# Kernel tuning notes

Measured on AMD Instinct MI355X. Metric: run time of the kernel, lower is better.

The kernel has to match this reference:

```python
import jax, jax.numpy as jnp
import numpy as np

B, N, C, H = 4, 2048, 1024, 16
D = C // H  # dim_per_head = 64
NEG = -1e9  # stands in for -inf masked_fill (finite to keep grads clean)


def setup_inputs() -> dict:
    key0 = jax.random.key(0)
    ks = jax.random.split(key0, 12)
    inp = {
        "query": jax.random.normal(ks[0], (B, N, C), dtype=jnp.float32),
        "key": jax.random.normal(ks[1], (B, N, C), dtype=jnp.float32),
        "value": jax.random.normal(ks[2], (B, N, C), dtype=jnp.float32),
        "ratio": jax.random.uniform(ks[3], (B, N), dtype=jnp.float32),
        "attn_mask": jax.random.randint(ks[4], (B, N, N), 0, 2) == 1,
        # learned params (Linear layers are bias-free; weights stored as [in, out])
        "Wq": jax.random.normal(ks[5], (C, C), dtype=jnp.float32) / np.sqrt(C),
        "Wk": jax.random.normal(ks[6], (C, C), dtype=jnp.float32) / np.sqrt(C),
        "Wv": jax.random.normal(ks[7], (C, C), dtype=jnp.float32) / np.sqrt(C),
        "Wo": jax.random.normal(ks[8], (C, C), dtype=jnp.float32) / np.sqrt(C),
        "gamma": jnp.ones((C,), dtype=jnp.float32),
        "beta": jnp.zeros((C,), dtype=jnp.float32),
    }
    return inp


def reference(query, key, value, ratio, attn_mask, Wq, Wk, Wv, Wo, gamma, beta):
    residual = query
    # projections -> [B, H, N, D]
    q = (query @ Wq).reshape(B, N, H, D).transpose(0, 2, 1, 3)
    k = (key @ Wk).reshape(B, N, H, D).transpose(0, 2, 1, 3)
    v = (value @ Wv).reshape(B, N, H, D).transpose(0, 2, 1, 3)

    scale = D ** (-0.5)
    scores = jnp.einsum("bhid,bhjd->bhij", q, k) * scale  # [B,H,N1,N2]
    scores = jnp.where(attn_mask[:, None, :, :], NEG, scores)
    scores = scores * ratio[:, None, None, :]  # ratio broadcast over heads & queries
    # NON-STANDARD: softmax over dim=2 (the QUERY axis), faithful to source
    attn = jax.nn.softmax(scores, axis=2)
    # dropout omitted (eval mode)
    ctx = jnp.einsum("bhij,bhjd->bhid", attn, v)  # [B,H,N1,D]
    ctx = ctx.transpose(0, 2, 1, 3).reshape(B, N, C)
    out = ctx @ Wo
    x = residual + out
    # LayerNorm over last dim
    mu = jnp.mean(x, axis=-1, keepdims=True)
    var = jnp.var(x, axis=-1, keepdims=True)
    xn = (x - mu) * jax.lax.rsqrt(var + 1e-5)
    return xn * gamma + beta
```

## Files before the change

kernel.cpp:

```cpp
#include <hip/hip_runtime.h>
#include <hip/hip_bf16.h>
#include <stdint.h>

#define BB 4
#define NN 2048
#define CC 1024
#define HH 16
#define DD 64

typedef __attribute__((ext_vector_type(8))) short bf16x8;
typedef __attribute__((ext_vector_type(4))) float f32x4;

#define LOG2E 1.44269504088896f

__device__ __forceinline__ float exp2_hw(float x) {
  float r;
  asm("v_exp_f32 %0, %1" : "=v"(r) : "v"(x));
  return r;
}
#define EXP2(x) exp2_hw(x)

__device__ __forceinline__ unsigned short f2bf(float x) {
  uint32_t u = __float_as_uint(x);
  uint32_t r = (u + 0x7FFFu + ((u >> 16) & 1u)) >> 16;
  return (unsigned short)r;
}
__device__ __forceinline__ float bf2f(unsigned short v) {
  return __uint_as_float(((uint32_t)v) << 16);
}
__device__ __forceinline__ float load_in_f(const void* p, size_t idx, int f32in) {
  if (f32in) return ((const float*)p)[idx];
  return bf2f(((const uint16_t*)p)[idx]);
}
__device__ __forceinline__ void gload16(uint16_t* lds_base, const uint16_t* gsrc) {
  __builtin_amdgcn_global_load_lds(
      (const __attribute__((address_space(1))) uint32_t*)(const void*)gsrc,
      (__attribute__((address_space(3))) uint32_t*)(void*)lds_base,
      16, 0, 0);
}

__global__ void detect_kernel(const uint32_t* __restrict__ q,
                              const uint32_t* __restrict__ m,
                              int* __restrict__ flags) {
  if (threadIdx.x == 0 && blockIdx.x == 0) {
    int sane = 0;
    for (int i = 0; i < 128; ++i) {
      uint32_t w = q[i];
      int e0 = (int)((w >> 7) & 0xFFu);
      int e1 = (int)((w >> 23) & 0xFFu);
      sane += (e0 >= 0x70 && e0 <= 0x8F) ? 1 : 0;
      sane += (e1 >= 0x70 && e1 <= 0x8F) ? 1 : 0;
    }
    flags[0] = (sane >= 208) ? 0 : 1;
    int allsmall = 1;
    for (int i = 0; i < 16; ++i) if (m[i] > 1u) allsmall = 0;
    flags[1] = allsmall;
  }
}

__global__ void conv_bf16_3(const void* __restrict__ s0, const void* __restrict__ s1,
                            const void* __restrict__ s2,
                            uint16_t* __restrict__ d0, uint16_t* __restrict__ d1,
                            uint16_t* __restrict__ d2,
                            int n, const int* __restrict__ flags) {
  const int f32in = flags[0];
  const void* src = (blockIdx.z == 0) ? s0 : (blockIdx.z == 1) ? s1 : s2;
  uint16_t* dst = (blockIdx.z == 0) ? d0 : (blockIdx.z == 1) ? d1 : d2;
  int idx = blockIdx.x * blockDim.x + threadIdx.x;
  const int total = n >> 2;
  const int stride = gridDim.x * blockDim.x;
  if (f32in) {
    const float4* s = (const float4*)src;
    for (; idx < total; idx += stride) {
      float4 v = s[idx];
      ushort4 o;
      o.x = f2bf(v.x); o.y = f2bf(v.y); o.z = f2bf(v.z); o.w = f2bf(v.w);
      ((ushort4*)dst)[idx] = o;
    }
  } else {
    const ushort4* s = (const ushort4*)src;
    for (; idx < total; idx += stride) ((ushort4*)dst)[idx] = s[idx];
  }
}

__global__ void conv_ratio2(const void* __restrict__ src, float* __restrict__ rs,
                            float* __restrict__ ng, int n, const int* __restrict__ flags) {
  const int f32in = flags[0];
  int idx = blockIdx.x * blockDim.x + threadIdx.x;
  const int stride = gridDim.x * blockDim.x;
  for (; idx < n; idx += stride) {
    float r = load_in_f(src, idx, f32in);
    rs[idx] = r * 0.125f * LOG2E;
    ng[idx] = r * (-1e9f) * LOG2E;
  }
}

__global__ void conv_maskbits(const void* __restrict__ src, uint32_t* __restrict__ dst,
                              int n, const int* __restrict__ flags) {
  const int isint = flags[1];
  const int gw = (blockIdx.x * blockDim.x + threadIdx.x) >> 6;
  const int lane = threadIdx.x & 63;
  const int nw = (gridDim.x * blockDim.x) >> 6;
  const int totalw = n >> 6;
  for (int w = gw; w < totalw; w += nw) {
    int e = w * 64 + lane;
    bool m;
    if (isint) m = (((const int*)src)[e] != 0);
    else       m = (((const uint8_t*)src)[e] != 0);
    unsigned long long bal = __ballot(m);
    if (lane == 0) ((unsigned long long*)dst)[w] = bal;
  }
}

__global__ __launch_bounds__(256)
void transW(const void* w0, const void* w1, const void* w2, const void* w3,
            uint16_t* __restrict__ wt, const int* __restrict__ flags) {
  const int f32in = flags[0];
  const void* src = (blockIdx.z == 0) ? w0 : (blockIdx.z == 1) ? w1
                   : (blockIdx.z == 2) ? w2 : w3;
  uint16_t* dst = wt + (size_t)blockIdx.z * CC * CC;
  __shared__ float t[32][33];
  const int tx = threadIdx.x, ty = threadIdx.y;
  const int n0 = blockIdx.x * 32, k0 = blockIdx.y * 32;
#pragma unroll
  for (int r = 0; r < 4; ++r) {
    int k = k0 + ty + r * 8;
    t[ty + r * 8][tx] = load_in_f(src, (size_t)k * CC + n0 + tx, f32in);
  }
  __syncthreads();
#pragma unroll
  for (int r = 0; r < 4; ++r) {
    int n = n0 + ty + r * 8;
    dst[(size_t)n * CC + k0 + tx] = f2bf(t[tx][ty + r * 8]);
  }
}

__global__ __launch_bounds__(256, 2)
void gemmQKV(const uint16_t* __restrict__ xq, const uint16_t* __restrict__ xk,
             const uint16_t* __restrict__ xv, const uint16_t* __restrict__ Wt,
             uint16_t* __restrict__ qb, uint16_t* __restrict__ kb,
             uint16_t* __restrict__ vtb, const float* __restrict__ rowscale) {
  __shared__ uint16_t As[128 * 32];
  __shared__ uint16_t Bs[128 * 32];
  const int tid = threadIdx.x;
  const int wid = tid >> 6, lane = tid & 63;
  const int g = lane >> 4, c = lane & 15;
  const int n0g = blockIdx.y * 128;
  const int sel = n0g >> 10;
  const int n0 = n0g & 1023;
  const int m0 = blockIdx.x * 128;
  const uint16_t* A = (sel == 0) ? xq : (sel == 1) ? xk : xv;
  const uint16_t* Bt = Wt + (size_t)sel * CC * CC;
  const int wr = wid >> 1, wc = wid & 1;
  f32x4 acc[4][4] = {};
  for (int k0 = 0; k0 < 1024; k0 += 32) {
    __syncthreads();
#pragma unroll
    for (int is = 0; is < 2; ++is) {
      int sb = is * 256 + wid * 64;
      int s = sb + lane;
      int r = s >> 2, kp = s & 3;
      int kps = kp ^ ((r >> 1) & 3);
      gload16(&As[sb * 8], A + (size_t)(m0 + r) * 1024 + k0 + kps * 8);
      gload16(&Bs[sb * 8], Bt + (size_t)(n0 + r) * 1024 + k0 + kps * 8);
    }
    __syncthreads();
    bf16x8 a[4], b[4];
#pragma unroll
    for (int mi = 0; mi < 4; ++mi) {
      int row = wr * 64 + mi * 16 + c;
      a[mi] = *(const bf16x8*)&As[row * 32 + (g ^ ((row >> 1) & 3)) * 8];
    }
#pragma unroll
    for (int ni = 0; ni < 4; ++ni) {
      int row = wc * 64 + ni * 16 + c;
      b[ni] = *(const bf16x8*)&Bs[row * 32 + (g ^ ((row >> 1) & 3)) * 8];
    }
#pragma unroll
    for (int mi = 0; mi < 4; ++mi)
#pragma unroll
      for (int ni = 0; ni < 4; ++ni)
        acc[mi][ni] = __builtin_amdgcn_mfma_f32_16x16x32_bf16(a[mi], b[ni], acc[mi][ni], 0, 0, 0);
  }
  float rsv[4][4];
  if (sel == 1) {
#pragma unroll
    for (int mi = 0; mi < 4; ++mi)
#pragma unroll
      for (int r = 0; r < 4; ++r)
        rsv[mi][r] = rowscale[m0 + wr * 64 + mi * 16 + g * 4 + r];
  }
#pragma unroll
  for (int mi = 0; mi < 4; ++mi)
#pragma unroll
    for (int ni = 0; ni < 4; ++ni)
#pragma unroll
      for (int r = 0; r < 4; ++r) {
        int mrow = m0 + wr * 64 + mi * 16 + g * 4 + r;
        int ncol = n0 + wc * 64 + ni * 16 + c;
        float v = acc[mi][ni][r];
        int b_ = mrow >> 11, i = mrow & 2047, h = ncol >> 6, d = ncol & 63;
        if (sel == 0) {
          qb[((size_t)(b_ * 16 + h) * 2048 + i) * 64 + d] = f2bf(v);
        } else if (sel == 1) {
          kb[((size_t)(b_ * 16 + h) * 2048 + i) * 64 + d] = f2bf(v * rsv[mi][r]);
        } else {
          vtb[((size_t)(b_ * 16 + h) * 64 + d) * 2048 + i] = f2bf(v);
        }
      }
}

__global__ __launch_bounds__(256, 2)
void gemmO(const uint16_t* __restrict__ A, const uint16_t* __restrict__ Bt,
           float* __restrict__ out, const void* __restrict__ resid,
           const int* __restrict__ flags) {
  __shared__ uint16_t As[128 * 32];
  __shared__ uint16_t Bs[128 * 32];
  const int tid = threadIdx.x;
  const int wid = tid >> 6, lane = tid & 63;
  const int g = lane >> 4, c = lane & 15;
  const int m0 = blockIdx.x * 128, n0 = blockIdx.y * 128;
  const int wr = wid >> 1, wc = wid & 1;
  f32x4 acc[4][4] = {};
  for (int k0 = 0; k0 < 1024; k0 += 32) {
    __syncthreads();
#pragma unroll
    for (int is = 0; is < 2; ++is) {
      int sb = is * 256 + wid * 64;
      int s = sb + lane;
      int r = s >> 2, kp = s & 3;
      int kps = kp ^ ((r >> 1) & 3);
      gload16(&As[sb * 8], A + (size_t)(m0 + r) * 1024 + k0 + kps * 8);
      gload16(&Bs[sb * 8], Bt + (size_t)(n0 + r) * 1024 + k0 + kps * 8);
    }
    __syncthreads();
    bf16x8 a[4], b[4];
#pragma unroll
    for (int mi = 0; mi < 4; ++mi) {
      int row = wr * 64 + mi * 16 + c;
      a[mi] = *(const bf16x8*)&As[row * 32 + (g ^ ((row >> 1) & 3)) * 8];
    }
#pragma unroll
    for (int ni = 0; ni < 4; ++ni) {
      int row = wc * 64 + ni * 16 + c;
      b[ni] = *(const bf16x8*)&Bs[row * 32 + (g ^ ((row >> 1) & 3)) * 8];
    }
#pragma unroll
    for (int mi = 0; mi < 4; ++mi)
#pragma unroll
      for (int ni = 0; ni < 4; ++ni)
        acc[mi][ni] = __builtin_amdgcn_mfma_f32_16x16x32_bf16(a[mi], b[ni], acc[mi][ni], 0, 0, 0);
  }
  const int f32in = flags[0];
#pragma unroll
  for (int mi = 0; mi < 4; ++mi)
#pragma unroll
    for (int ni = 0; ni < 4; ++ni)
#pragma unroll
      for (int r = 0; r < 4; ++r) {
        int mrow = m0 + wr * 64 + mi * 16 + g * 4 + r;
        int ncol = n0 + wc * 64 + ni * 16 + c;
        size_t idx = (size_t)mrow * 1024 + ncol;
        out[idx] = acc[mi][ni][r] + load_in_f(resid, idx, f32in);
      }
}

__global__ __launch_bounds__(256, 2)
void attn_stats(const uint16_t* __restrict__ qb, const uint16_t* __restrict__ kb,
                uint16_t* __restrict__ vt, const uint32_t* __restrict__ mbits,
                const float* __restrict__ ngbuf) {
  __shared__ float redL[4][128];
  __shared__ float invsh[128];
  const int tid = threadIdx.x, wid = tid >> 6, lane = tid & 63;
  const int g = lane >> 4, c = lane & 15;
  const int bh = blockIdx.x, b_ = bh >> 4;
  const int j0 = blockIdx.y * 128;
  const uint16_t* Kg = kb + (size_t)bh * NN * DD + (size_t)j0 * DD;
  const uint16_t* Qg = qb + (size_t)bh * NN * DD;
  const uint32_t* Mrow = mbits + (size_t)b_ * NN * 64 + (j0 >> 5);
  bf16x8 kf[2][8];
#pragma unroll
  for (int ks = 0; ks < 2; ++ks)
#pragma unroll
    for (int nj = 0; nj < 8; ++nj)
      kf[ks][nj] = *(const bf16x8*)(Kg + (size_t)(nj * 16 + c) * 64 + ks * 32 + g * 8);
  float ng8[8], l_[8];
#pragma unroll
  for (int nj = 0; nj < 8; ++nj) {
    ng8[nj] = ngbuf[b_ * NN + j0 + nj * 16 + c];
    l_[nj] = 0.f;
  }
  bf16x8 qa[2][2], qn[2][2];
  uint4 mqa[8], mqb[8];
#pragma unroll
  for (int ks = 0; ks < 2; ++ks)
#pragma unroll
    for (int mi = 0; mi < 2; ++mi)
      qa[ks][mi] = *(const bf16x8*)(Qg + (size_t)(wid * 32 + mi * 16 + c) * 64 + ks * 32 + g * 8);
#pragma unroll
  for (int u = 0; u < 8; ++u) {
    int mi = u >> 2, r = u & 3;
    mqa[u] = *(const uint4*)(Mrow + (size_t)(wid * 32 + mi * 16 + g * 4 + r) * 64);
  }

  auto body = [&](bf16x8 (&qc)[2][2], bf16x8 (&qp)[2][2],
                  uint4 (&mc)[8], uint4 (&mn)[8], int i0) {
    f32x4 sacc[2][8] = {};
    __builtin_amdgcn_s_setprio(1);
#pragma unroll
    for (int ks = 0; ks < 2; ++ks)
#pragma unroll
      for (int mi = 0; mi < 2; ++mi)
#pragma unroll
        for (int nj = 0; nj < 8; ++nj)
          sacc[mi][nj] = __builtin_amdgcn_mfma_f32_16x16x32_bf16(qc[ks][mi], kf[ks][nj], sacc[mi][nj], 0, 0, 0);
    __builtin_amdgcn_s_setprio(0);
    int ip = (i0 + 128) & (NN - 1);
#pragma unroll
    for (int ks = 0; ks < 2; ++ks)
#pragma unroll
      for (int mi = 0; mi < 2; ++mi)
        qp[ks][mi] = *(const bf16x8*)(Qg + (size_t)(ip + wid * 32 + mi * 16 + c) * 64 + ks * 32 + g * 8);
#pragma unroll
    for (int u = 0; u < 8; ++u) {
      int mi = u >> 2, r = u & 3;
      mn[u] = *(const uint4*)(Mrow + (size_t)(ip + wid * 32 + mi * 16 + g * 4 + r) * 64);
    }
#pragma unroll
    for (int mi = 0; mi < 2; ++mi)
#pragma unroll
      for (int r = 0; r < 4; ++r) {
        const uint4 mw = mc[mi * 4 + r];
#pragma unroll
        for (int nj = 0; nj < 8; ++nj) {
          uint32_t w = (nj < 2) ? mw.x : (nj < 4) ? mw.y : (nj < 6) ? mw.z : mw.w;
          bool bit = (w >> ((nj & 1) * 16 + c)) & 1u;
          float se = bit ? ng8[nj] : sacc[mi][nj][r];
          l_[nj] += EXP2(se);
        }
      }
  };
  for (int it = 0; it < 8; ++it) {
    body(qa, qn, mqa, mqb, it * 256);
    body(qn, qa, mqb, mqa, it * 256 + 128);
  }
#pragma unroll
  for (int nj = 0; nj < 8; ++nj) {
    float l = l_[nj];
    l += __shfl_xor(l, 16);
    l += __shfl_xor(l, 32);
    if (g == 0) redL[wid][nj * 16 + c] = l;
  }
  __syncthreads();
  if (tid < 128) {
    float L = redL[0][tid] + redL[1][tid] + redL[2][tid] + redL[3][tid];
    invsh[tid] = 1.0f / L;
  }
  __syncthreads();
  {
    const int d = tid >> 2, jseg = (tid & 3) * 32;
    uint16_t* vrow = vt + (size_t)bh * DD * NN + (size_t)d * NN + j0 + jseg;
#pragma unroll
    for (int u = 0; u < 4; ++u) {
      bf16x8 v = *(const bf16x8*)(vrow + u * 8);
      bf16x8 o;
#pragma unroll
      for (int e = 0; e < 8; ++e) {
        float f = bf2f((unsigned short)v[e]) * invsh[jseg + u * 8 + e];
        o[e] = (short)f2bf(f);
      }
      *(bf16x8*)(vrow + u * 8) = o;
    }
  }
}

__global__ __launch_bounds__(256, 3)
void attn_pv(const uint16_t* __restrict__ qb, const uint16_t* __restrict__ kb,
             const uint16_t* __restrict__ vt, const uint32_t* __restrict__ mbits,
             const float* __restrict__ ngbuf, uint16_t* __restrict__ ctxr) {
  __shared__ uint16_t Ks[2][64 * 64];
  __shared__ uint16_t Vs[2][64 * 64];
  __shared__ uint16_t Ps[128 * 64];
  const int tid = threadIdx.x, wid = tid >> 6, lane = tid & 63;
  const int g = lane >> 4, c = lane & 15;
  const int bh = blockIdx.x, b_ = bh >> 4, h = bh & 15;
  const int i0 = blockIdx.y * 128;
  const uint16_t* Qg = qb + (size_t)bh * NN * DD;
  const uint16_t* Kg = kb + (size_t)bh * NN * DD;
  const uint16_t* Vg = vt + (size_t)bh * DD * NN;
  const uint32_t* Mb = mbits + (size_t)b_ * NN * 64;
  const float* ngb = ngbuf + b_ * NN;

  auto stageK = [&](int buf, int j0) {
#pragma unroll
    for (int is = 0; is < 2; ++is) {
      int sb = is * 256 + wid * 64;
      int s = sb + lane;
      int row = s >> 3, gr = s & 7;
      gload16(&Ks[buf][sb * 8], Kg + (size_t)(j0 + row) * 64 + (gr ^ (row & 7)) * 8);
    }
  };
  auto stageV = [&](int buf, int j0) {
#pragma unroll
    for (int is = 0; is < 2; ++is) {
      int sb = is * 256 + wid * 64;
      int s = sb + lane;
      int d = s >> 3, gr = s & 7;
      gload16(&Vs[buf][sb * 8], Vg + (size_t)d * NN + j0 + (gr ^ (d & 7)) * 8);
    }
  };

  bf16x8 qf[2][2];
#pragma unroll
  for (int ks = 0; ks < 2; ++ks)
#pragma unroll
    for (int mi = 0; mi < 2; ++mi)
      qf[ks][mi] = *(const bf16x8*)(Qg + (size_t)(i0 + wid * 32 + mi * 16 + c) * 64 + ks * 32 + g * 8);

  stageK(0, 0); stageV(0, 0);
  __syncthreads();

  f32x4 cacc[2][4] = {};
  for (int t = 0; t < 32; ++t) {
    const int j0 = t * 64, cb = t & 1, nb = cb ^ 1;
    if (t < 31) { stageK(nb, j0 + 64); stageV(nb, j0 + 64); }
    uint2 mw0 = *(const uint2*)(Mb + (size_t)(i0 + wid * 32 + c) * 64 + (j0 >> 5));
    uint2 mw1 = *(const uint2*)(Mb + (size_t)(i0 + wid * 32 + 16 + c) * 64 + (j0 >> 5));
    float4 ngv[4];
#pragma unroll
    for (int nj = 0; nj < 4; ++nj)
      ngv[nj] = *(const float4*)(ngb + j0 + nj * 16 + g * 4);
    f32x4 st[4][2] = {};
    __builtin_amdgcn_s_setprio(1);
#pragma unroll
    for (int ks = 0; ks < 2; ++ks) {
      bf16x8 kfr[4];
#pragma unroll
      for (int nj = 0; nj < 4; ++nj) {
        int row = nj * 16 + c;
        kfr[nj] = *(const bf16x8*)&Ks[cb][row * 64 + (((ks * 4 + g) ^ (c & 7))) * 8];
      }
#pragma unroll
      for (int nj = 0; nj < 4; ++nj)
#pragma unroll
        for (int mi = 0; mi < 2; ++mi)
          st[nj][mi] = __builtin_amdgcn_mfma_f32_16x16x32_bf16(kfr[nj], qf[ks][mi], st[nj][mi], 0, 0, 0);
    }
    __builtin_amdgcn_s_setprio(0);
    uint2 pkv[4][2];
#pragma unroll
    for (int nj = 0; nj < 4; ++nj) {
      const float4 ngq = ngv[nj];
      float nz[4] = {ngq.x, ngq.y, ngq.z, ngq.w};
#pragma unroll
      for (int mi = 0; mi < 2; ++mi) {
        const uint2 mw = mi ? mw1 : mw0;
        uint32_t w = (nj < 2) ? mw.x : mw.y;
        float p[4];
#pragma unroll
        for (int u = 0; u < 4; ++u) {
          bool bit = (w >> ((nj & 1) * 16 + g * 4 + u)) & 1u;
          float se = bit ? nz[u] : st[nj][mi][u];
          p[u] = EXP2(se);
        }
        uint32_t lo, hi;
        asm("v_cvt_pk_bf16_f32 %0, %1, %2" : "=v"(lo) : "v"(p[0]), "v"(p[1]));
        asm("v_cvt_pk_bf16_f32 %0, %1, %2" : "=v"(hi) : "v"(p[2]), "v"(p[3]));
        pkv[nj][mi] = make_uint2(lo, hi);
      }
    }
#pragma unroll
    for (int nj = 0; nj < 4; ++nj)
#pragma unroll
      for (int mi = 0; mi < 2; ++mi) {
        int iL = wid * 32 + mi * 16 + c;
        int gran = (nj * 2 + (g >> 1)) ^ (c & 7);
        *(uint2*)((char*)Ps + iL * 128 + gran * 16 + (g & 1) * 8) = pkv[nj][mi];
      }
    __syncthreads();
    __builtin_amdgcn_s_setprio(1);
#pragma unroll
    for (int ks = 0; ks < 2; ++ks) {
      bf16x8 pa[2], vb[4];
#pragma unroll
      for (int mi = 0; mi < 2; ++mi) {
        int row = wid * 32 + mi * 16 + c;
        pa[mi] = *(const bf16x8*)((const char*)Ps + row * 128 + (((ks * 4 + g) ^ (c & 7))) * 16);
      }
#pragma unroll
      for (int nd = 0; nd < 4; ++nd) {
        int row = nd * 16 + c;
        vb[nd] = *(const bf16x8*)&Vs[cb][row * 64 + (((ks * 4 + g) ^ (c & 7))) * 8];
      }
#pragma unroll
      for (int mi = 0; mi < 2; ++mi)
#pragma unroll
        for (int nd = 0; nd < 4; ++nd)
          cacc[mi][nd] = __builtin_amdgcn_mfma_f32_16x16x32_bf16(pa[mi], vb[nd], cacc[mi][nd], 0, 0, 0);
    }
    __builtin_amdgcn_s_setprio(0);
    __syncthreads();
  }
#pragma unroll
  for (int mi = 0; mi < 2; ++mi)
#pragma unroll
    for (int nd = 0; nd < 4; ++nd)
#pragma unroll
      for (int r = 0; r < 4; ++r) {
        int i = i0 + wid * 32 + mi * 16 + g * 4 + r;
        int d = nd * 16 + c;
        ctxr[((size_t)(b_ * NN + i)) * CC + h * DD + d] = f2bf(cacc[mi][nd][r]);
      }
}

__global__ __launch_bounds__(256)
void ln_kernel(const float* __restrict__ xbuf, const void* __restrict__ gamma,
               const void* __restrict__ beta, float* __restrict__ out,
               const int* __restrict__ flags) {
  const int row = blockIdx.x;
  const int tid = threadIdx.x;
  const float4 v = ((const float4*)(xbuf + (size_t)row * CC))[tid];
  float s = v.x + v.y + v.z + v.w;
  float s2 = v.x * v.x + v.y * v.y + v.z * v.z + v.w * v.w;
#pragma unroll
  for (int off = 32; off >= 1; off >>= 1) {
    s += __shfl_xor(s, off);
    s2 += __shfl_xor(s2, off);
  }
  __shared__ float red[8];
  const int wid = tid >> 6, lane = tid & 63;
  if (lane == 0) { red[wid] = s; red[4 + wid] = s2; }
  __syncthreads();
  float ts = red[0] + red[1] + red[2] + red[3];
  float ts2 = red[4] + red[5] + red[6] + red[7];
  float mu = ts * (1.f / 1024.f);
  float var = ts2 * (1.f / 1024.f) - mu * mu;
  float rs = rsqrtf(var + 1e-5f);
  const int f32in = flags[0];
  const int cbase = tid * 4;
  float4 o;
  o.x = (v.x - mu) * rs * load_in_f(gamma, cbase + 0, f32in) + load_in_f(beta, cbase + 0, f32in);
  o.y = (v.y - mu) * rs * load_in_f(gamma, cbase + 1, f32in) + load_in_f(beta, cbase + 1, f32in);
  o.z = (v.z - mu) * rs * load_in_f(gamma, cbase + 2, f32in) + load_in_f(beta, cbase + 2, f32in);
  o.w = (v.w - mu) * rs * load_in_f(gamma, cbase + 3, f32in) + load_in_f(beta, cbase + 3, f32in);
  ((float4*)(out + (size_t)row * CC))[tid] = o;
}

extern "C" void kernel_launch(void* const* d_in, const int* in_sizes, int n_in,
                              void* d_out, int out_size, void* d_ws, size_t ws_size,
                              hipStream_t stream) {
  (void)in_sizes; (void)n_in; (void)out_size; (void)ws_size;
  char* ws = (char*)d_ws;
  size_t off = 0;
  auto alloc = [&](size_t bytes) -> void* {
    void* p = ws + off;
    off += (bytes + 255) & ~(size_t)255;
    return p;
  };
  int*      flags   = (int*)alloc(256);
  float*    rsbuf   = (float*)alloc((size_t)BB * NN * 4);
  float*    ngbuf   = (float*)alloc((size_t)BB * NN * 4);
  uint32_t* mbits   = (uint32_t*)alloc((size_t)BB * NN * 64 * 4);
  uint16_t* xq      = (uint16_t*)alloc((size_t)BB * NN * CC * 2);
  uint16_t* xk      = (uint16_t*)alloc((size_t)BB * NN * CC * 2);
  uint16_t* xv      = (uint16_t*)alloc((size_t)BB * NN * CC * 2);
  uint16_t* qb      = (uint16_t*)alloc((size_t)BB * NN * CC * 2);
  uint16_t* kb      = (uint16_t*)alloc((size_t)BB * NN * CC * 2);
  uint16_t* vtb     = (uint16_t*)alloc((size_t)BB * NN * CC * 2);
  uint16_t* Wt      = (uint16_t*)alloc((size_t)4 * CC * CC * 2);
  uint16_t* ctxr    = xq;
  float*    xbuf    = (float*)xk;

  detect_kernel<<<1, 64, 0, stream>>>((const uint32_t*)d_in[0], (const uint32_t*)d_in[4], flags);
  conv_bf16_3<<<dim3(2048, 1, 3), 256, 0, stream>>>(d_in[0], d_in[1], d_in[2],
                                                    xq, xk, xv, BB * NN * CC, flags);
  conv_ratio2<<<32, 256, 0, stream>>>(d_in[3], rsbuf, ngbuf, BB * NN, flags);
  conv_maskbits<<<2048, 256, 0, stream>>>(d_in[4], mbits, BB * NN * NN, flags);
  transW<<<dim3(32, 32, 4), dim3(32, 8), 0, stream>>>(d_in[5], d_in[6], d_in[7], d_in[8], Wt, flags);

  gemmQKV<<<dim3(64, 24), 256, 0, stream>>>(xq, xk, xv, Wt, qb, kb, vtb, rsbuf);

  attn_stats<<<dim3(64, 16), 256, 0, stream>>>(qb, kb, vtb, mbits, ngbuf);
  attn_pv<<<dim3(64, 16), 256, 0, stream>>>(qb, kb, vtb, mbits, ngbuf, ctxr);

  gemmO<<<dim3(64, 8), 256, 0, stream>>>(ctxr, Wt + 3 * CC * CC, xbuf, d_in[0], flags);
  ln_kernel<<<8192, 256, 0, stream>>>(xbuf, d_in[9], d_in[10], (float*)d_out, flags);
}
```

Baseline: 417.4 us.

## Stage K tile in LDS for attn_stats and merge prep kernels into one launch

In attn_stats, the K fragments that were held in registers for the whole block are now loaded once into a swizzled LDS tile and re-read per k-step. The mask-word prefetch double buffer is replaced by loads issued at the start of each iteration. Together these cut register pressure so launch bounds can rise from 2 to 3 blocks per SIMD for more latency hiding. The cost is extra LDS reads each iteration and mask loads that are no longer prefetched a step ahead. Separately, the bf16 conversion, ratio and mask-bit preprocessing kernels are fused into a single launch split by blockIdx.z to cut launch overhead; the ratio slice launches 2048 blocks although only 32 have work.

Result: slower. 616.7 us (+47.7%).

```diff
diff --git a/kernel.cpp b/kernel.cpp
--- a/kernel.cpp
+++ b/kernel.cpp
@@ -58,57 +58,55 @@
   }
 }
 
-__global__ void conv_bf16_3(const void* __restrict__ s0, const void* __restrict__ s1,
-                            const void* __restrict__ s2,
+__global__ void prep_kernel(const void* __restrict__ s0, const void* __restrict__ s1,
+                            const void* __restrict__ s2, const void* __restrict__ ratio,
+                            const void* __restrict__ mask,
                             uint16_t* __restrict__ d0, uint16_t* __restrict__ d1,
                             uint16_t* __restrict__ d2,
-                            int n, const int* __restrict__ flags) {
-  const int f32in = flags[0];
-  const void* src = (blockIdx.z == 0) ? s0 : (blockIdx.z == 1) ? s1 : s2;
-  uint16_t* dst = (blockIdx.z == 0) ? d0 : (blockIdx.z == 1) ? d1 : d2;
-  int idx = blockIdx.x * blockDim.x + threadIdx.x;
-  const int total = n >> 2;
-  const int stride = gridDim.x * blockDim.x;
-  if (f32in) {
-    const float4* s = (const float4*)src;
-    for (; idx < total; idx += stride) {
-      float4 v = s[idx];
-      ushort4 o;
-      o.x = f2bf(v.x); o.y = f2bf(v.y); o.z = f2bf(v.z); o.w = f2bf(v.w);
-      ((ushort4*)dst)[idx] = o;
+                            float* __restrict__ rs, float* __restrict__ ng,
+                            uint32_t* __restrict__ mb, const int* __restrict__ flags) {
+  const int z = blockIdx.z;
+  if (z < 3) {
+    const int f32in = flags[0];
+    const void* src = (z == 0) ? s0 : (z == 1) ? s1 : s2;
+    uint16_t* dst = (z == 0) ? d0 : (z == 1) ? d1 : d2;
+    int idx = blockIdx.x * blockDim.x + threadIdx.x;
+    const int total = (BB * NN * CC) >> 2;
+    const int stride = gridDim.x * blockDim.x;
+    if (f32in) {
+      const float4* s = (const float4*)src;
+      for (; idx < total; idx += stride) {
+        float4 v = s[idx];
+        ushort4 o;
+        o.x = f2bf(v.x); o.y = f2bf(v.y); o.z = f2bf(v.z); o.w = f2bf(v.w);
+        ((ushort4*)dst)[idx] = o;
+      }
+    } else {
+      const ushort4* s = (const ushort4*)src;
+      for (; idx < total; idx += stride) ((ushort4*)dst)[idx] = s[idx];
+    }
+  } else if (z == 3) {
+    const int isint = flags[1];
+    const int gw = (blockIdx.x * blockDim.x + threadIdx.x) >> 6;
+    const int lane = threadIdx.x & 63;
+    const int nw = (gridDim.x * blockDim.x) >> 6;
+    const int totalw = (BB * NN * NN) >> 6;
+    for (int w = gw; w < totalw; w += nw) {
+      int e = w * 64 + lane;
+      bool m;
+      if (isint) m = (((const int*)mask)[e] != 0);
+      else       m = (((const uint8_t*)mask)[e] != 0);
+      unsigned long long bal = __ballot(m);
+      if (lane == 0) ((unsigned long long*)mb)[w] = bal;
     }
   } else {
-    const ushort4* s = (const ushort4*)src;
-    for (; idx < total; idx += stride) ((ushort4*)dst)[idx] = s[idx];
-  }
-}
-
-__global__ void conv_ratio2(const void* __restrict__ src, float* __restrict__ rs,
-                            float* __restrict__ ng, int n, const int* __restrict__ flags) {
-  const int f32in = flags[0];
-  int idx = blockIdx.x * blockDim.x + threadIdx.x;
-  const int stride = gridDim.x * blockDim.x;
-  for (; idx < n; idx += stride) {
-    float r = load_in_f(src, idx, f32in);
-    rs[idx] = r * 0.125f * LOG2E;
-    ng[idx] = r * (-1e9f) * LOG2E;
-  }
-}
-
-__global__ void conv_maskbits(const void* __restrict__ src, uint32_t* __restrict__ dst,
-                              int n, const int* __restrict__ flags) {
-  const int isint = flags[1];
-  const int gw = (blockIdx.x * blockDim.x + threadIdx.x) >> 6;
-  const int lane = threadIdx.x & 63;
-  const int nw = (gridDim.x * blockDim.x) >> 6;
-  const int totalw = n >> 6;
-  for (int w = gw; w < totalw; w += nw) {
-    int e = w * 64 + lane;
-    bool m;
-    if (isint) m = (((const int*)src)[e] != 0);
-    else       m = (((const uint8_t*)src)[e] != 0);
-    unsigned long long bal = __ballot(m);
-    if (lane == 0) ((unsigned long long*)dst)[w] = bal;
+    const int f32in = flags[0];
+    int idx = blockIdx.x * blockDim.x + threadIdx.x;
+    if (idx < BB * NN) {
+      float r = load_in_f(ratio, idx, f32in);
+      rs[idx] = r * 0.125f * LOG2E;
+      ng[idx] = r * (-1e9f) * LOG2E;
+    }
   }
 }
 
@@ -265,10 +263,11 @@
       }
 }
 
-__global__ __launch_bounds__(256, 2)
+__global__ __launch_bounds__(256, 3)
 void attn_stats(const uint16_t* __restrict__ qb, const uint16_t* __restrict__ kb,
                 uint16_t* __restrict__ vt, const uint32_t* __restrict__ mbits,
                 const float* __restrict__ ngbuf) {
+  __shared__ uint16_t Ks[128 * 64];
   __shared__ float redL[4][128];
   __shared__ float invsh[128];
   const int tid = threadIdx.x, wid = tid >> 6, lane = tid & 63;
@@ -278,12 +277,13 @@
   const uint16_t* Kg = kb + (size_t)bh * NN * DD + (size_t)j0 * DD;
   const uint16_t* Qg = qb + (size_t)bh * NN * DD;
   const uint32_t* Mrow = mbits + (size_t)b_ * NN * 64 + (j0 >> 5);
-  bf16x8 kf[2][8];
-#pragma unroll
-  for (int ks = 0; ks < 2; ++ks)
-#pragma unroll
-    for (int nj = 0; nj < 8; ++nj)
-      kf[ks][nj] = *(const bf16x8*)(Kg + (size_t)(nj * 16 + c) * 64 + ks * 32 + g * 8);
+#pragma unroll
+  for (int is = 0; is < 4; ++is) {
+    int sb = is * 256 + wid * 64;
+    int s = sb + lane;
+    int row = s >> 3, gr = s & 7;
+    gload16(&Ks[sb * 8], Kg + (size_t)row * 64 + (gr ^ (row & 7)) * 8);
+  }
   float ng8[8], l_[8];
 #pragma unroll
   for (int nj = 0; nj < 8; ++nj) {
@@ -291,29 +291,36 @@
     l_[nj] = 0.f;
   }
   bf16x8 qa[2][2], qn[2][2];
-  uint4 mqa[8], mqb[8];
 #pragma unroll
   for (int ks = 0; ks < 2; ++ks)
 #pragma unroll
     for (int mi = 0; mi < 2; ++mi)
       qa[ks][mi] = *(const bf16x8*)(Qg + (size_t)(wid * 32 + mi * 16 + c) * 64 + ks * 32 + g * 8);
-#pragma unroll
-  for (int u = 0; u < 8; ++u) {
-    int mi = u >> 2, r = u & 3;
-    mqa[u] = *(const uint4*)(Mrow + (size_t)(wid * 32 + mi * 16 + g * 4 + r) * 64);
-  }
-
-  auto body = [&](bf16x8 (&qc)[2][2], bf16x8 (&qp)[2][2],
-                  uint4 (&mc)[8], uint4 (&mn)[8], int i0) {
+  __syncthreads();
+
+  auto body = [&](bf16x8 (&qc)[2][2], bf16x8 (&qp)[2][2], int i0) {
+    uint4 mq[8];
+#pragma unroll
+    for (int u = 0; u < 8; ++u) {
+      int mi = u >> 2, r = u & 3;
+      mq[u] = *(const uint4*)(Mrow + (size_t)(i0 + wid * 32 + mi * 16 + g * 4 + r) * 64);
+    }
     f32x4 sacc[2][8] = {};
     __builtin_amdgcn_s_setprio(1);
 #pragma unroll
-    for (int ks = 0; ks < 2; ++ks)
+    for (int ks = 0; ks < 2; ++ks) {
+      bf16x8 kfr[8];
+#pragma unroll
+      for (int nj = 0; nj < 8; ++nj) {
+        int row = nj * 16 + c;
+        kfr[nj] = *(const bf16x8*)&Ks[row * 64 + (((ks * 4 + g) ^ (row & 7))) * 8];
+      }
 #pragma unroll
       for (int mi = 0; mi < 2; ++mi)
 #pragma unroll
         for (int nj = 0; nj < 8; ++nj)
-          sacc[mi][nj] = __builtin_amdgcn_mfma_f32_16x16x32_bf16(qc[ks][mi], kf[ks][nj], sacc[mi][nj], 0, 0, 0);
+          sacc[mi][nj] = __builtin_amdgcn_mfma_f32_16x16x32_bf16(qc[ks][mi], kfr[nj], sacc[mi][nj], 0, 0, 0);
+    }
     __builtin_amdgcn_s_setprio(0);
     int ip = (i0 + 128) & (NN - 1);
 #pragma unroll
@@ -322,15 +329,10 @@
       for (int mi = 0; mi < 2; ++mi)
         qp[ks][mi] = *(const bf16x8*)(Qg + (size_t)(ip + wid * 32 + mi * 16 + c) * 64 + ks * 32 + g * 8);
 #pragma unroll
-    for (int u = 0; u < 8; ++u) {
-      int mi = u >> 2, r = u & 3;
-      mn[u] = *(const uint4*)(Mrow + (size_t)(ip + wid * 32 + mi * 16 + g * 4 + r) * 64);
-    }
-#pragma unroll
     for (int mi = 0; mi < 2; ++mi)
 #pragma unroll
       for (int r = 0; r < 4; ++r) {
-        const uint4 mw = mc[mi * 4 + r];
+        const uint4 mw = mq[mi * 4 + r];
 #pragma unroll
         for (int nj = 0; nj < 8; ++nj) {
           uint32_t w = (nj < 2) ? mw.x : (nj < 4) ? mw.y : (nj < 6) ? mw.z : mw.w;
@@ -341,8 +343,8 @@
       }
   };
   for (int it = 0; it < 8; ++it) {
-    body(qa, qn, mqa, mqb, it * 256);
-    body(qn, qa, mqb, mqa, it * 256 + 128);
+    body(qa, qn, it * 256);
+    body(qn, qa, it * 256 + 128);
   }
 #pragma unroll
   for (int nj = 0; nj < 8; ++nj) {
@@ -572,10 +574,8 @@
   float*    xbuf    = (float*)xk;
 
   detect_kernel<<<1, 64, 0, stream>>>((const uint32_t*)d_in[0], (const uint32_t*)d_in[4], flags);
-  conv_bf16_3<<<dim3(2048, 1, 3), 256, 0, stream>>>(d_in[0], d_in[1], d_in[2],
-                                                    xq, xk, xv, BB * NN * CC, flags);
-  conv_ratio2<<<32, 256, 0, stream>>>(d_in[3], rsbuf, ngbuf, BB * NN, flags);
-  conv_maskbits<<<2048, 256, 0, stream>>>(d_in[4], mbits, BB * NN * NN, flags);
+  prep_kernel<<<dim3(2048, 1, 5), 256, 0, stream>>>(d_in[0], d_in[1], d_in[2], d_in[3], d_in[4],
+                                                    xq, xk, xv, rsbuf, ngbuf, mbits, flags);
   transW<<<dim3(32, 32, 4), dim3(32, 8), 0, stream>>>(d_in[5], d_in[6], d_in[7], d_in[8], Wt, flags);
 
   gemmQKV<<<dim3(64, 24), 256, 0, stream>>>(xq, xk, xv, Wt, qb, kb, vtb, rsbuf);
```
